# Kernel optimization log

Measured on AMD Instinct MI355X. Metric: run time of the kernel, lower is better.

## Reference

```python
import jax, jax.numpy as jnp
import numpy as np

E_DIM = 1024
HID = 4096
H = (2 * HID) // 3  # floor(2*hidden/3) = 2730
NUM_EXPERTS = 8
TOP_K = 2
LN_EPS = 1e-5


def setup_inputs() -> dict:
    key = jax.random.key(0)
    ks = jax.random.split(key, 10)
    B, T, P = 2, 8, 256
    s_in = 1.0 / np.sqrt(E_DIM)
    s_h = 1.0 / np.sqrt(H)
    return {
        "x": jax.random.normal(ks[0], (B, T, P, E_DIM), jnp.float32),
        "Wr": jax.random.normal(ks[1], (NUM_EXPERTS, E_DIM), jnp.float32) * s_in,
        "Wv": jax.random.normal(ks[2], (NUM_EXPERTS, E_DIM, H), jnp.float32) * s_in,
        "bv": jax.random.normal(ks[3], (NUM_EXPERTS, H), jnp.float32) * 0.01,
        "Wg": jax.random.normal(ks[4], (NUM_EXPERTS, E_DIM, H), jnp.float32) * s_in,
        "bg": jax.random.normal(ks[5], (NUM_EXPERTS, H), jnp.float32) * 0.01,
        "Wo": jax.random.normal(ks[6], (NUM_EXPERTS, H, E_DIM), jnp.float32) * s_h,
        "bo": jax.random.normal(ks[7], (NUM_EXPERTS, E_DIM), jnp.float32) * 0.01,
        "ln_g": jnp.ones((E_DIM,), jnp.float32),
        "ln_b": jnp.zeros((E_DIM,), jnp.float32),
    }


def reference(x, Wr, Wv, bv, Wg, bg, Wo, bo, ln_g, ln_b):
    B, T, P, E = x.shape
    flat = x.reshape(-1, E)          # [N, E]
    N = flat.shape[0]

    # router: top-k logits -> softmax combine weights
    logits = flat @ Wr.T                              # [N, C]
    tk_vals, tk_idx = jax.lax.top_k(logits, TOP_K)    # [N, K]
    tk_w = jax.nn.softmax(tk_vals, axis=-1)           # [N, K]

    # dense combine-weight matrix: zero for non-routed experts
    comb = jnp.zeros((N, NUM_EXPERTS), flat.dtype)
    comb = comb.at[jnp.arange(N)[:, None], tk_idx].add(tk_w)  # [N, C]

    # all experts over all tokens (masked combine makes this exact)
    hv = jnp.einsum('ne,ceh->cnh', flat, Wv) + bv[:, None, :]  # [C, N, H]
    hg = jnp.einsum('ne,ceh->cnh', flat, Wg) + bg[:, None, :]
    h = jax.nn.silu(hv) * hg                                   # SwiGLU
    oe = jnp.einsum('cnh,che->cne', h, Wo) + bo[:, None, :]    # [C, N, E]
    out = jnp.einsum('cne,nc->ne', oe, comb)                   # weighted combine

    # residual + LayerNorm (AdaptiveNormalizer with no conditioning)
    y = x + out.reshape(B, T, P, E)
    mu = jnp.mean(y, axis=-1, keepdims=True)
    var = jnp.mean((y - mu) ** 2, axis=-1, keepdims=True)
    return ln_g * (y - mu) * jax.lax.rsqrt(var + LN_EPS) + ln_b
```

## Files before the change

kernel.cpp:

```cpp
#include <hip/hip_runtime.h>
#include <hip/hip_bf16.h>

#define E_DIM 1024
#define HDIM  2730
#define HP    2816
#define NEXP  8
#define NTOK  4096
#define NPAIR 8192
#define NSLOT 72
#define LN_EPS 1e-5f

typedef __attribute__((ext_vector_type(8))) short  short8;
typedef __attribute__((ext_vector_type(4))) short  short4v;
typedef __attribute__((ext_vector_type(4))) float  floatx4;
typedef __attribute__((ext_vector_type(4))) int    intx4;

__device__ __forceinline__ __hip_bfloat16 f2bf(float f) { return __float2bfloat16(f); }

__device__ __forceinline__ void gload16(const __hip_bfloat16* g, __hip_bfloat16* l) {
  __builtin_amdgcn_global_load_lds(
      (const __attribute__((address_space(1))) void*)(g),
      (__attribute__((address_space(3))) void*)(l), 16, 0, 0);
}

__global__ __launch_bounds__(256) void router_k(const float* __restrict__ x,
    const float* __restrict__ Wr, int* __restrict__ counts,
    int* __restrict__ tk_idx, float* __restrict__ tk_w) {
  int wid = threadIdx.x >> 6, lane = threadIdx.x & 63;
  int t = blockIdx.x * 4 + wid;
  const float* xr = x + (size_t)t * E_DIM;
  float xv[16];
#pragma unroll
  for (int i = 0; i < 16; ++i) xv[i] = xr[lane + 64 * i];
  float lg[8];
#pragma unroll
  for (int e = 0; e < 8; ++e) {
    const float* wr = Wr + e * E_DIM;
    float a = 0.f;
#pragma unroll
    for (int i = 0; i < 16; ++i) a += xv[i] * wr[lane + 64 * i];
#pragma unroll
    for (int o = 32; o; o >>= 1) a += __shfl_xor(a, o, 64);
    lg[e] = a;
  }
  if (lane == 0) {
    int i0 = 0; float l0 = lg[0];
#pragma unroll
    for (int e = 1; e < 8; ++e) if (lg[e] > l0) { l0 = lg[e]; i0 = e; }
    int i1 = -1; float l1 = -1e30f;
#pragma unroll
    for (int e = 0; e < 8; ++e) if (e != i0 && lg[e] > l1) { l1 = lg[e]; i1 = e; }
    float w0 = 1.f / (1.f + __expf(l1 - l0));
    atomicAdd(&counts[i0], 1);
    atomicAdd(&counts[i1], 1);
    tk_idx[2 * t]     = i0;  tk_idx[2 * t + 1] = i1;
    tk_w[2 * t]       = w0;  tk_w[2 * t + 1]   = 1.f - w0;
  }
}

__global__ void offsets_k(const int* __restrict__ counts, int* __restrict__ offsets,
                          int* __restrict__ cursor,
                          int* __restrict__ slot_e, int* __restrict__ slot_m0) {
  if (threadIdx.x == 0) {
    int off = 0, s = 0;
    for (int e = 0; e < NEXP; ++e) {
      offsets[e] = off; cursor[e] = off;
      for (int m0 = 0; m0 < counts[e]; m0 += 128) { slot_e[s] = e; slot_m0[s] = m0; ++s; }
      off += counts[e];
    }
    for (; s < NSLOT; ++s) { slot_e[s] = -1; slot_m0[s] = 0; }
  }
}

__global__ __launch_bounds__(256) void scatter_k(const int* __restrict__ tk_idx,
    const float* __restrict__ tk_w, int* __restrict__ cursor,
    int* __restrict__ pair_token, float* __restrict__ pair_w, int* __restrict__ pair_pos) {
  int t = blockIdx.x * 256 + threadIdx.x;
#pragma unroll
  for (int k = 0; k < 2; ++k) {
    int e = tk_idx[2 * t + k];
    int pos = atomicAdd(&cursor[e], 1);
    pair_token[pos] = t;
    pair_w[pos] = tk_w[2 * t + k];
    pair_pos[2 * t + k] = pos;
  }
}

__global__ __launch_bounds__(256) void gatherx_k(const float* __restrict__ x,
    const int* __restrict__ pair_token, __hip_bfloat16* __restrict__ xs) {
  int p = blockIdx.x;
  int t = pair_token[p];
  const float* src = x + (size_t)t * E_DIM;
  __hip_bfloat16* dst = xs + (size_t)p * E_DIM;
  int i = threadIdx.x * 4;
  floatx4 v = *(const floatx4*)(src + i);
  union { __hip_bfloat16 h[4]; short4v s; } u;
#pragma unroll
  for (int j = 0; j < 4; ++j) u.h[j] = f2bf(v[j]);
  *(short4v*)(dst + i) = u.s;
}

__global__ __launch_bounds__(256) void tcvt_k(const float* __restrict__ in,
    __hip_bfloat16* __restrict__ out, int R, int C, int outRS,
    size_t inExpStride, size_t outExpStride) {
  __shared__ float tile[64 * 65];
  int e = blockIdx.z;
  const float* ip = in + inExpStride * e;
  __hip_bfloat16* op = out + outExpStride * e;
  int c0 = blockIdx.x * 64, r0 = blockIdx.y * 64;
#pragma unroll
  for (int i = 0; i < 16; ++i) {
    int idx = i * 256 + threadIdx.x;
    int rr = idx >> 6, cc = idx & 63;
    int gr = r0 + rr, gc = c0 + cc;
    tile[rr * 65 + cc] = (gr < R && gc < C) ? ip[(size_t)gr * C + gc] : 0.f;
  }
  __syncthreads();
#pragma unroll
  for (int i = 0; i < 2; ++i) {
    int idx = i * 256 + threadIdx.x;
    int cc = idx >> 3, rb = (idx & 7) * 8;
    union { __hip_bfloat16 h[8]; intx4 v; } u;
#pragma unroll
    for (int j = 0; j < 8; ++j) u.h[j] = f2bf(tile[(rb + j) * 65 + cc]);
    *(intx4*)(op + (size_t)(c0 + cc) * outRS + (r0 + rb)) = u.v;
  }
}

__global__ __launch_bounds__(256, 2) void gemm1_k(
    const __hip_bfloat16* __restrict__ xs,
    const int* __restrict__ counts, const int* __restrict__ offsets,
    const int* __restrict__ slot_e, const int* __restrict__ slot_m0,
    const float* __restrict__ bv, const float* __restrict__ bg,
    const __hip_bfloat16* __restrict__ WvT, const __hip_bfloat16* __restrict__ WgT,
    __hip_bfloat16* __restrict__ h) {
  int slot = blockIdx.y;
  int e = slot_e[slot];
  if (e < 0) return;
  int m0 = slot_m0[slot];
  int Me = counts[e], off = offsets[e];
  int n0 = blockIdx.x * 128;

  __shared__ __align__(16) __hip_bfloat16 sA[2][128 * 32];
  __shared__ __align__(16) __hip_bfloat16 sBv[2][128 * 32];
  __shared__ __align__(16) __hip_bfloat16 sBg[2][128 * 32];

  int tid = threadIdx.x;
  int wid = tid >> 6, lane = tid & 63;
  int wm = wid >> 1, wn = wid & 1;
  int q = lane >> 4, r = lane & 15;

  int csw = (q ^ ((r >> 1) & 3)) << 3;
  int aoff[4], boff[4];
#pragma unroll
  for (int mi = 0; mi < 4; ++mi) aoff[mi] = (wm * 64 + mi * 16 + r) * 32 + csw;
#pragma unroll
  for (int ni = 0; ni < 4; ++ni) boff[ni] = (wn * 64 + ni * 16 + r) * 32 + csw;

  int srow4   = lane >> 2;
  int schunk4 = (lane & 3) ^ ((lane >> 3) & 3);
  const __hip_bfloat16* gA = xs + (size_t)(off + m0 + wid * 16 + srow4) * E_DIM + schunk4 * 8;
  size_t wb = (size_t)e * ((size_t)HP * E_DIM);
  size_t browoff = wb + (size_t)(n0 + wid * 16 + srow4) * E_DIM + schunk4 * 8;
  const __hip_bfloat16* gv = WvT + browoff;
  const __hip_bfloat16* gg = WgT + browoff;

  floatx4 accv[4][4], accg[4][4];
  floatx4 zz = {0.f, 0.f, 0.f, 0.f};
#pragma unroll
  for (int mi = 0; mi < 4; ++mi)
#pragma unroll
    for (int ni = 0; ni < 4; ++ni) { accv[mi][ni] = zz; accg[mi][ni] = zz; }

#define G1_STAGE(BUF)                                                          \
  {                                                                            \
    _Pragma("unroll")                                                          \
    for (int i = 0; i < 2; ++i) {                                              \
      gload16(gA + (size_t)i * 64 * E_DIM, &sA[BUF][(wid + i * 4) * 512]);     \
      gload16(gv + (size_t)i * 64 * E_DIM, &sBv[BUF][(wid + i * 4) * 512]);    \
      gload16(gg + (size_t)i * 64 * E_DIM, &sBg[BUF][(wid + i * 4) * 512]);    \
    }                                                                          \
    gA += 32; gv += 32; gg += 32;                                              \
  }

#define G1_COMPUTE(BUF)                                                        \
  {                                                                            \
    short8 av[4];                                                              \
    _Pragma("unroll")                                                          \
    for (int mi = 0; mi < 4; ++mi)                                             \
      av[mi] = *(const short8*)(&sA[BUF][aoff[mi]]);                           \
    _Pragma("unroll")                                                          \
    for (int ni = 0; ni < 4; ++ni) {                                           \
      short8 b8v = *(const short8*)(&sBv[BUF][boff[ni]]);                      \
      short8 b8g = *(const short8*)(&sBg[BUF][boff[ni]]);                      \
      _Pragma("unroll")                                                        \
      for (int mi = 0; mi < 4; ++mi) {                                         \
        accv[mi][ni] = __builtin_amdgcn_mfma_f32_16x16x32_bf16(av[mi], b8v, accv[mi][ni], 0, 0, 0); \
        accg[mi][ni] = __builtin_amdgcn_mfma_f32_16x16x32_bf16(av[mi], b8g, accg[mi][ni], 0, 0, 0); \
      }                                                                        \
    }                                                                          \
  }

  G1_STAGE(0);
  __syncthreads();
  for (int kt = 0; kt < E_DIM / 32 - 2; kt += 2) {
    G1_STAGE(1);
    G1_COMPUTE(0);
    __syncthreads();
    G1_STAGE(0);
    G1_COMPUTE(1);
    __syncthreads();
  }
  G1_STAGE(1);
  G1_COMPUTE(0);
  __syncthreads();
  G1_COMPUTE(1);

  float bvv[4], bgv[4];
#pragma unroll
  for (int ni = 0; ni < 4; ++ni) {
    int n = n0 + wn * 64 + ni * 16 + r;
    bvv[ni] = (n < HDIM) ? bv[e * HDIM + n] : 0.f;
    bgv[ni] = (n < HDIM) ? bg[e * HDIM + n] : 0.f;
  }
#pragma unroll
  for (int mi = 0; mi < 4; ++mi) {
#pragma unroll
    for (int rr = 0; rr < 4; ++rr) {
      int m_loc = wm * 64 + mi * 16 + q * 4 + rr;
      int m = m0 + m_loc;
      if (m >= Me) continue;
      size_t hrow = (size_t)(off + m) * HP;
#pragma unroll
      for (int ni = 0; ni < 4; ++ni) {
        int n = n0 + wn * 64 + ni * 16 + r;
        float hv = accv[mi][ni][rr] + bvv[ni];
        float hg = accg[mi][ni][rr] + bgv[ni];
        float sgm = 1.f / (1.f + __expf(-hv));
        h[hrow + n] = f2bf(hv * sgm * hg);
      }
    }
  }
}

__global__ __launch_bounds__(256, 2) void gemm2_k(
    const __hip_bfloat16* __restrict__ hb,
    const int* __restrict__ counts, const int* __restrict__ offsets,
    const int* __restrict__ slot_e, const int* __restrict__ slot_m0,
    const float* __restrict__ bo,
    const __hip_bfloat16* __restrict__ WoT,
    float* __restrict__ pout) {
  int slot = blockIdx.y;
  int e = slot_e[slot];
  if (e < 0) return;
  int m0 = slot_m0[slot];
  int Me = counts[e], off = offsets[e];
  int n0 = blockIdx.x * 128;

  __shared__ __align__(16) __hip_bfloat16 sA[2][128 * 32];
  __shared__ __align__(16) __hip_bfloat16 sB[2][128 * 32];

  int tid = threadIdx.x;
  int wid = tid >> 6, lane = tid & 63;
  int wm = wid >> 1, wn = wid & 1;
  int q = lane >> 4, r = lane & 15;

  int csw = (q ^ ((r >> 1) & 3)) << 3;
  int aoff[4], boff[4];
#pragma unroll
  for (int mi = 0; mi < 4; ++mi) aoff[mi] = (wm * 64 + mi * 16 + r) * 32 + csw;
#pragma unroll
  for (int ni = 0; ni < 4; ++ni) boff[ni] = (wn * 64 + ni * 16 + r) * 32 + csw;

  int srow4   = lane >> 2;
  int schunk4 = (lane & 3) ^ ((lane >> 3) & 3);
  const __hip_bfloat16* gA = hb + (size_t)(off + m0 + wid * 16 + srow4) * HP + schunk4 * 8;
  const __hip_bfloat16* gB = WoT + (size_t)e * ((size_t)E_DIM * HP) +
                             (size_t)(n0 + wid * 16 + srow4) * HP + schunk4 * 8;

  floatx4 acc[4][4];
  floatx4 zz = {0.f, 0.f, 0.f, 0.f};
#pragma unroll
  for (int mi = 0; mi < 4; ++mi)
#pragma unroll
    for (int ni = 0; ni < 4; ++ni) acc[mi][ni] = zz;

#define G2_STAGE(BUF)                                                          \
  {                                                                            \
    _Pragma("unroll")                                                          \
    for (int i = 0; i < 2; ++i) {                                              \
      gload16(gA + (size_t)i * 64 * HP, &sA[BUF][(wid + i * 4) * 512]);        \
      gload16(gB + (size_t)i * 64 * HP, &sB[BUF][(wid + i * 4) * 512]);        \
    }                                                                          \
    gA += 32; gB += 32;                                                        \
  }

#define G2_COMPUTE(BUF)                                                        \
  {                                                                            \
    short8 av[4];                                                              \
    _Pragma("unroll")                                                          \
    for (int mi = 0; mi < 4; ++mi)                                             \
      av[mi] = *(const short8*)(&sA[BUF][aoff[mi]]);                           \
    _Pragma("unroll")                                                          \
    for (int ni = 0; ni < 4; ++ni) {                                           \
      short8 b8 = *(const short8*)(&sB[BUF][boff[ni]]);                        \
      _Pragma("unroll")                                                        \
      for (int mi = 0; mi < 4; ++mi)                                           \
        acc[mi][ni] = __builtin_amdgcn_mfma_f32_16x16x32_bf16(av[mi], b8, acc[mi][ni], 0, 0, 0); \
    }                                                                          \
  }

  G2_STAGE(0);
  __syncthreads();
  for (int kt = 0; kt < HP / 32 - 2; kt += 2) {
    G2_STAGE(1);
    G2_COMPUTE(0);
    __syncthreads();
    G2_STAGE(0);
    G2_COMPUTE(1);
    __syncthreads();
  }
  G2_STAGE(1);
  G2_COMPUTE(0);
  __syncthreads();
  G2_COMPUTE(1);

#pragma unroll
  for (int mi = 0; mi < 4; ++mi) {
#pragma unroll
    for (int rr = 0; rr < 4; ++rr) {
      int m_loc = wm * 64 + mi * 16 + q * 4 + rr;
      int m = m0 + m_loc;
      if (m >= Me) continue;
      size_t orow = (size_t)(off + m) * E_DIM;
#pragma unroll
      for (int ni = 0; ni < 4; ++ni) {
        int n = n0 + wn * 64 + ni * 16 + r;
        pout[orow + n] = acc[mi][ni][rr] + bo[e * E_DIM + n];
      }
    }
  }
}

__global__ __launch_bounds__(256) void ln_k(const float* __restrict__ x,
    const float* __restrict__ pout, const int* __restrict__ pair_pos,
    const float* __restrict__ pair_w, const float* __restrict__ ln_g,
    const float* __restrict__ ln_b, float* __restrict__ out) {
  int t = blockIdx.x, tid = threadIdx.x;
  int p0 = pair_pos[2 * t], p1 = pair_pos[2 * t + 1];
  float w0 = pair_w[p0], w1 = pair_w[p1];
  const float* xr = x + (size_t)t * E_DIM;
  const float* r0 = pout + (size_t)p0 * E_DIM;
  const float* r1 = pout + (size_t)p1 * E_DIM;
  float y[4];
  float s = 0.f, ss = 0.f;
#pragma unroll
  for (int i = 0; i < 4; ++i) {
    int e = tid + 256 * i;
    y[i] = xr[e] + w0 * r0[e] + w1 * r1[e];
    s += y[i];
    ss += y[i] * y[i];
  }
#pragma unroll
  for (int o = 32; o; o >>= 1) { s += __shfl_xor(s, o, 64); ss += __shfl_xor(ss, o, 64); }
  __shared__ float red[8];
  int wid = tid >> 6, lane = tid & 63;
  if (lane == 0) { red[wid] = s; red[4 + wid] = ss; }
  __syncthreads();
  s  = red[0] + red[1] + red[2] + red[3];
  ss = red[4] + red[5] + red[6] + red[7];
  float mu = s * (1.f / E_DIM);
  float var = ss * (1.f / E_DIM) - mu * mu;
  float rs = rsqrtf(var + LN_EPS);
#pragma unroll
  for (int i = 0; i < 4; ++i) {
    int e = tid + 256 * i;
    out[(size_t)t * E_DIM + e] = ln_g[e] * (y[i] - mu) * rs + ln_b[e];
  }
}

extern "C" void kernel_launch(void* const* d_in, const int* in_sizes, int n_in,
                              void* d_out, int out_size, void* d_ws, size_t ws_size,
                              hipStream_t stream) {
  const float* x    = (const float*)d_in[0];
  const float* Wr   = (const float*)d_in[1];
  const float* Wv   = (const float*)d_in[2];
  const float* bv   = (const float*)d_in[3];
  const float* Wg   = (const float*)d_in[4];
  const float* bg   = (const float*)d_in[5];
  const float* Wo   = (const float*)d_in[6];
  const float* bo   = (const float*)d_in[7];
  const float* ln_g = (const float*)d_in[8];
  const float* ln_b = (const float*)d_in[9];
  float* out = (float*)d_out;

  char* ws = (char*)d_ws;
  size_t off = 0;
  auto alloc = [&](size_t bytes) -> void* {
    void* p = ws + off;
    off = (off + bytes + 255) & ~(size_t)255;
    return p;
  };
  int*   counts     = (int*)alloc(32);
  int*   cursor     = (int*)alloc(32);
  int*   offsets    = (int*)alloc(32);
  int*   slot_e     = (int*)alloc(NSLOT * 4);
  int*   slot_m0    = (int*)alloc(NSLOT * 4);
  int*   tk_idx     = (int*)alloc((size_t)NTOK * 2 * 4);
  float* tk_w       = (float*)alloc((size_t)NTOK * 2 * 4);
  int*   pair_token = (int*)alloc((size_t)NPAIR * 4);
  float* pair_w     = (float*)alloc((size_t)NPAIR * 4);
  int*   pair_pos   = (int*)alloc((size_t)NPAIR * 4);
  __hip_bfloat16* xs   = (__hip_bfloat16*)alloc((size_t)(NPAIR + 128) * E_DIM * 2);
  __hip_bfloat16* hbuf = (__hip_bfloat16*)alloc((size_t)(NPAIR + 128) * HP * 2);
  float* pout = (float*)alloc((size_t)NPAIR * E_DIM * 4);

  size_t welems = (size_t)NEXP * HP * E_DIM;
  __hip_bfloat16* WvT = (__hip_bfloat16*)alloc(welems * 2);
  __hip_bfloat16* WgT = (__hip_bfloat16*)alloc(welems * 2);
  __hip_bfloat16* WoT = (__hip_bfloat16*)alloc(welems * 2);

  hipMemsetAsync(d_ws, 0, 1024, stream);

  router_k<<<NTOK / 4, 256, 0, stream>>>(x, Wr, counts, tk_idx, tk_w);
  offsets_k<<<1, 64, 0, stream>>>(counts, offsets, cursor, slot_e, slot_m0);
  scatter_k<<<NTOK / 256, 256, 0, stream>>>(tk_idx, tk_w, cursor, pair_token, pair_w, pair_pos);
  gatherx_k<<<NPAIR, 256, 0, stream>>>(x, pair_token, xs);

  tcvt_k<<<dim3(HP / 64, E_DIM / 64, NEXP), 256, 0, stream>>>(
      Wv, WvT, E_DIM, HDIM, E_DIM, (size_t)E_DIM * HDIM, (size_t)HP * E_DIM);
  tcvt_k<<<dim3(HP / 64, E_DIM / 64, NEXP), 256, 0, stream>>>(
      Wg, WgT, E_DIM, HDIM, E_DIM, (size_t)E_DIM * HDIM, (size_t)HP * E_DIM);
  tcvt_k<<<dim3(E_DIM / 64, HP / 64, NEXP), 256, 0, stream>>>(
      Wo, WoT, HDIM, E_DIM, HP, (size_t)HDIM * E_DIM, (size_t)E_DIM * HP);

  gemm1_k<<<dim3(HP / 128, NSLOT), 256, 0, stream>>>(
      xs, counts, offsets, slot_e, slot_m0, bv, bg, WvT, WgT, hbuf);
  gemm2_k<<<dim3(E_DIM / 128, NSLOT), 256, 0, stream>>>(
      hbuf, counts, offsets, slot_e, slot_m0, bo, WoT, pout);

  ln_k<<<NTOK, 256, 0, stream>>>(x, pout, pair_pos, pair_w, ln_g, ln_b, out);
}
```

Baseline: 729.8 us.

## Triple-buffer expert GEMM K-loops with partial vmcnt waits and MFMA priority

Both grouped expert GEMMs move from double-buffered LDS staging with full __syncthreads to a three-buffer ring. Each step issues the next tile's global-to-LDS loads, then waits only until the older tile has arrived (partial vmcnt) and hits a raw barrier, so two tiles can be in flight while one is computed. LDS fragments are loaded up front and the MFMA block runs at raised wave priority. The cost is more LDS per block (gemm1 grows to about 72KB), which can limit residency at the requested two blocks per CU, and the hand-counted waitcnt values must match the number of loads issued per stage.

```diff
diff --git a/kernel.cpp b/kernel.cpp
--- a/kernel.cpp
+++ b/kernel.cpp
@@ -9,6 +9,7 @@
 #define NPAIR 8192
 #define NSLOT 72
 #define LN_EPS 1e-5f
+#define BUFH  (128 * 32)
 
 typedef __attribute__((ext_vector_type(8))) short  short8;
 typedef __attribute__((ext_vector_type(4))) short  short4v;
@@ -22,6 +23,11 @@
       (const __attribute__((address_space(1))) void*)(g),
       (__attribute__((address_space(3))) void*)(l), 16, 0, 0);
 }
+
+#define VMC6 do { asm volatile("s_waitcnt vmcnt(6)" ::: "memory"); __builtin_amdgcn_sched_barrier(0); } while (0)
+#define VMC4 do { asm volatile("s_waitcnt vmcnt(4)" ::: "memory"); __builtin_amdgcn_sched_barrier(0); } while (0)
+#define VMC0 do { asm volatile("s_waitcnt vmcnt(0)" ::: "memory"); __builtin_amdgcn_sched_barrier(0); } while (0)
+#define BAR  __builtin_amdgcn_s_barrier()
 
 __global__ __launch_bounds__(256) void router_k(const float* __restrict__ x,
     const float* __restrict__ Wr, int* __restrict__ counts,
@@ -141,9 +147,9 @@
   int Me = counts[e], off = offsets[e];
   int n0 = blockIdx.x * 128;
 
-  __shared__ __align__(16) __hip_bfloat16 sA[2][128 * 32];
-  __shared__ __align__(16) __hip_bfloat16 sBv[2][128 * 32];
-  __shared__ __align__(16) __hip_bfloat16 sBg[2][128 * 32];
+  __shared__ __align__(16) __hip_bfloat16 sA[3 * BUFH];
+  __shared__ __align__(16) __hip_bfloat16 sBv[3 * BUFH];
+  __shared__ __align__(16) __hip_bfloat16 sBg[3 * BUFH];
 
   int tid = threadIdx.x;
   int wid = tid >> 6, lane = tid & 63;
@@ -172,49 +178,50 @@
 #pragma unroll
     for (int ni = 0; ni < 4; ++ni) { accv[mi][ni] = zz; accg[mi][ni] = zz; }
 
-#define G1_STAGE(BUF)                                                          \
-  {                                                                            \
-    _Pragma("unroll")                                                          \
-    for (int i = 0; i < 2; ++i) {                                              \
-      gload16(gA + (size_t)i * 64 * E_DIM, &sA[BUF][(wid + i * 4) * 512]);     \
-      gload16(gv + (size_t)i * 64 * E_DIM, &sBv[BUF][(wid + i * 4) * 512]);    \
-      gload16(gg + (size_t)i * 64 * E_DIM, &sBg[BUF][(wid + i * 4) * 512]);    \
-    }                                                                          \
-    gA += 32; gv += 32; gg += 32;                                              \
-  }
-
-#define G1_COMPUTE(BUF)                                                        \
-  {                                                                            \
-    short8 av[4];                                                              \
-    _Pragma("unroll")                                                          \
-    for (int mi = 0; mi < 4; ++mi)                                             \
-      av[mi] = *(const short8*)(&sA[BUF][aoff[mi]]);                           \
-    _Pragma("unroll")                                                          \
-    for (int ni = 0; ni < 4; ++ni) {                                           \
-      short8 b8v = *(const short8*)(&sBv[BUF][boff[ni]]);                      \
-      short8 b8g = *(const short8*)(&sBg[BUF][boff[ni]]);                      \
-      _Pragma("unroll")                                                        \
-      for (int mi = 0; mi < 4; ++mi) {                                         \
-        accv[mi][ni] = __builtin_amdgcn_mfma_f32_16x16x32_bf16(av[mi], b8v, accv[mi][ni], 0, 0, 0); \
-        accg[mi][ni] = __builtin_amdgcn_mfma_f32_16x16x32_bf16(av[mi], b8g, accg[mi][ni], 0, 0, 0); \
-      }                                                                        \
-    }                                                                          \
-  }
-
-  G1_STAGE(0);
-  __syncthreads();
-  for (int kt = 0; kt < E_DIM / 32 - 2; kt += 2) {
-    G1_STAGE(1);
-    G1_COMPUTE(0);
-    __syncthreads();
-    G1_STAGE(0);
-    G1_COMPUTE(1);
-    __syncthreads();
-  }
-  G1_STAGE(1);
-  G1_COMPUTE(0);
-  __syncthreads();
-  G1_COMPUTE(1);
+#define G1_STAGE(C, KK)                                                         \
+  {                                                                             \
+    size_t _ko = (size_t)(KK) * 32;                                             \
+    _Pragma("unroll")                                                           \
+    for (int i = 0; i < 2; ++i) {                                               \
+      gload16(gA + _ko + (size_t)i * 64 * E_DIM, &sA[(C) * BUFH + (wid + i * 4) * 512]);  \
+      gload16(gv + _ko + (size_t)i * 64 * E_DIM, &sBv[(C) * BUFH + (wid + i * 4) * 512]); \
+      gload16(gg + _ko + (size_t)i * 64 * E_DIM, &sBg[(C) * BUFH + (wid + i * 4) * 512]); \
+    }                                                                           \
+  }
+
+#define G1_COMP(C)                                                              \
+  {                                                                             \
+    short8 av[4], b8v[4], b8g[4];                                               \
+    _Pragma("unroll")                                                           \
+    for (int mi = 0; mi < 4; ++mi)                                              \
+      av[mi] = *(const short8*)(&sA[(C) * BUFH + aoff[mi]]);                    \
+    _Pragma("unroll")                                                           \
+    for (int ni = 0; ni < 4; ++ni) {                                            \
+      b8v[ni] = *(const short8*)(&sBv[(C) * BUFH + boff[ni]]);                  \
+      b8g[ni] = *(const short8*)(&sBg[(C) * BUFH + boff[ni]]);                  \
+    }                                                                           \
+    __builtin_amdgcn_s_setprio(1);                                              \
+    _Pragma("unroll")                                                           \
+    for (int ni = 0; ni < 4; ++ni)                                              \
+      _Pragma("unroll")                                                         \
+      for (int mi = 0; mi < 4; ++mi) {                                          \
+        accv[mi][ni] = __builtin_amdgcn_mfma_f32_16x16x32_bf16(av[mi], b8v[ni], accv[mi][ni], 0, 0, 0); \
+        accg[mi][ni] = __builtin_amdgcn_mfma_f32_16x16x32_bf16(av[mi], b8g[ni], accg[mi][ni], 0, 0, 0); \
+      }                                                                         \
+    __builtin_amdgcn_s_setprio(0);                                              \
+  }
+
+  G1_STAGE(0, 0);
+  G1_STAGE(1, 1);
+  VMC6; BAR;
+
+  for (int kt = 0; kt < 30; kt += 3) {
+    G1_STAGE(2, kt + 2); G1_COMP(0); VMC6; BAR;
+    G1_STAGE(0, kt + 3); G1_COMP(1); VMC6; BAR;
+    G1_STAGE(1, kt + 4); G1_COMP(2); VMC6; BAR;
+  }
+  G1_COMP(0); VMC0; BAR;
+  G1_COMP(1);
 
   float bvv[4], bgv[4];
 #pragma unroll
@@ -257,8 +264,8 @@
   int Me = counts[e], off = offsets[e];
   int n0 = blockIdx.x * 128;
 
-  __shared__ __align__(16) __hip_bfloat16 sA[2][128 * 32];
-  __shared__ __align__(16) __hip_bfloat16 sB[2][128 * 32];
+  __shared__ __align__(16) __hip_bfloat16 sA[3 * BUFH];
+  __shared__ __align__(16) __hip_bfloat16 sB[3 * BUFH];
 
   int tid = threadIdx.x;
   int wid = tid >> 6, lane = tid & 63;
@@ -285,45 +292,47 @@
 #pragma unroll
     for (int ni = 0; ni < 4; ++ni) acc[mi][ni] = zz;
 
-#define G2_STAGE(BUF)                                                          \
-  {                                                                            \
-    _Pragma("unroll")                                                          \
-    for (int i = 0; i < 2; ++i) {                                              \
-      gload16(gA + (size_t)i * 64 * HP, &sA[BUF][(wid + i * 4) * 512]);        \
-      gload16(gB + (size_t)i * 64 * HP, &sB[BUF][(wid + i * 4) * 512]);        \
-    }                                                                          \
-    gA += 32; gB += 32;                                                        \
-  }
-
-#define G2_COMPUTE(BUF)                                                        \
-  {                                                                            \
-    short8 av[4];                                                              \
-    _Pragma("unroll")                                                          \
-    for (int mi = 0; mi < 4; ++mi)                                             \
-      av[mi] = *(const short8*)(&sA[BUF][aoff[mi]]);                           \
-    _Pragma("unroll")                                                          \
-    for (int ni = 0; ni < 4; ++ni) {                                           \
-      short8 b8 = *(const short8*)(&sB[BUF][boff[ni]]);                        \
-      _Pragma("unroll")                                                        \
-      for (int mi = 0; mi < 4; ++mi)                                           \
-        acc[mi][ni] = __builtin_amdgcn_mfma_f32_16x16x32_bf16(av[mi], b8, acc[mi][ni], 0, 0, 0); \
-    }                                                                          \
-  }
-
-  G2_STAGE(0);
-  __syncthreads();
-  for (int kt = 0; kt < HP / 32 - 2; kt += 2) {
-    G2_STAGE(1);
-    G2_COMPUTE(0);
-    __syncthreads();
-    G2_STAGE(0);
-    G2_COMPUTE(1);
-    __syncthreads();
-  }
-  G2_STAGE(1);
-  G2_COMPUTE(0);
-  __syncthreads();
-  G2_COMPUTE(1);
+#define G2_STAGE(C, KK)                                                         \
+  {                                                                             \
+    size_t _ko = (size_t)(KK) * 32;                                             \
+    _Pragma("unroll")                                                           \
+    for (int i = 0; i < 2; ++i) {                                               \
+      gload16(gA + _ko + (size_t)i * 64 * HP, &sA[(C) * BUFH + (wid + i * 4) * 512]); \
+      gload16(gB + _ko + (size_t)i * 64 * HP, &sB[(C) * BUFH + (wid + i * 4) * 512]); \
+    }                                                                           \
+  }
+
+#define G2_COMP(C)                                                              \
+  {                                                                             \
+    short8 av[4], b8[4];                                                        \
+    _Pragma("unroll")                                                           \
+    for (int mi = 0; mi < 4; ++mi)                                              \
+      av[mi] = *(const short8*)(&sA[(C) * BUFH + aoff[mi]]);                    \
+    _Pragma("unroll")                                                           \
+    for (int ni = 0; ni < 4; ++ni)                                              \
+      b8[ni] = *(const short8*)(&sB[(C) * BUFH + boff[ni]]);                    \
+    __builtin_amdgcn_s_setprio(1);                                              \
+    _Pragma("unroll")                                                           \
+    for (int ni = 0; ni < 4; ++ni)                                              \
+      _Pragma("unroll")                                                         \
+      for (int mi = 0; mi < 4; ++mi)                                            \
+        acc[mi][ni] = __builtin_amdgcn_mfma_f32_16x16x32_bf16(av[mi], b8[ni], acc[mi][ni], 0, 0, 0); \
+    __builtin_amdgcn_s_setprio(0);                                              \
+  }
+
+  G2_STAGE(0, 0);
+  G2_STAGE(1, 1);
+  VMC4; BAR;
+
+  for (int kt = 0; kt < 84; kt += 3) {
+    G2_STAGE(2, kt + 2); G2_COMP(0); VMC4; BAR;
+    G2_STAGE(0, kt + 3); G2_COMP(1); VMC4; BAR;
+    G2_STAGE(1, kt + 4); G2_COMP(2); VMC4; BAR;
+  }
+  G2_STAGE(2, 86); G2_COMP(0); VMC4; BAR;
+  G2_STAGE(0, 87); G2_COMP(1); VMC4; BAR;
+  G2_COMP(2); VMC0; BAR;
+  G2_COMP(0);
 
 #pragma unroll
   for (int mi = 0; mi < 4; ++mi) {
```

New measurement: 711.1 us. -2.6%, faster.
